# Kernel tuning notes

Hardware: AMD Instinct MI355X
Metric: run time of the kernel (lower is better)

Reference implementation:

```python
import jax, jax.numpy as jnp
import numpy as np

ALPHA = 1.0
NEG = -1e20  # matches torch code's -1e+20 padding for impossible cells


def setup_inputs() -> dict:
    key = jax.random.key(0)
    W = jax.random.normal(key, (32, 512, 1024), dtype=jnp.float32)
    return {"W": W}


def _combine(x, y):
    # associative operator for the log-space linear recurrence
    # m_j = logaddexp(m_{j-1} + a_j, b_j)
    a1, b1 = x
    a2, b2 = y
    return (a1 + a2, jnp.logaddexp(b1 + a2, b2))


def _forward(W):
    # Faithful to BayesianDTW.compute_location / compute_location_new:
    #   mu[:,0,:] = mu[:,:,0] = -1e20, mu[:,0,0] = 0
    #   mu[i,j] = logsumexp(mu[i-1,j], mu[i,j-1], mu[i-1,j-1]) + alpha*W[i-1,j-1]
    # Implemented as a row scan; the within-row left-neighbor dependency is a
    # log-space linear recurrence solved with an associative scan (O(Na*log Nb)
    # depth instead of O(Na*Nb) sequential steps).
    B, Na, Nb = W.shape
    aW = ALPHA * W  # [B, Na, Nb]
    row0 = jnp.concatenate(
        [jnp.zeros((B, 1), W.dtype), jnp.full((B, Nb), NEG, W.dtype)], axis=1
    )  # mu[:, 0, :]

    def step(prev_row, w_row):
        # prev_row: mu[:, i-1, :] -> [B, Nb+1]; w_row: alpha*W[:, i-1, :] -> [B, Nb]
        c = jnp.logaddexp(prev_row[:, 1:], prev_row[:, :-1])  # top + top-left
        # mu[i,j] = logaddexp(mu[i,j-1] + w_j, c_j + w_j), mu[i,0] = NEG
        A, Bc = jax.lax.associative_scan(_combine, (w_row, c + w_row), axis=1)
        m = jnp.logaddexp(NEG + A, Bc)  # include mu[i,0] = NEG initial carry
        new_row = jnp.concatenate(
            [jnp.full((m.shape[0], 1), NEG, m.dtype), m], axis=1
        )
        return new_row, new_row

    _, rows = jax.lax.scan(step, row0, jnp.transpose(aW, (1, 0, 2)))  # [Na, B, Nb+1]
    mu = jnp.concatenate([row0[:, None, :], jnp.transpose(rows, (1, 0, 2))], axis=1)
    return mu  # [B, Na+1, Nb+1], scale=False behavior


def reference(W):
    return _forward(W)
```

## Files before the change

### kernel.cpp

```cpp
#include <hip/hip_runtime.h>
#include <stdint.h>
#include <stddef.h>


#define NBATCH  32
#define NA      512
#define NB      1024
#define NSTRIPE 8
#define SW      128
#define CH      8
#define NCHUNK  (NA / CH)
#define LSTR    128
#define OROWS   513
#define OCOLS   1025
#define FSTRIDE 32

#define NEGV    (-1e20f)
#define LOG2E   (1.4426950408889634f)
#define LN2     (0.6931471805599453f)
#define NEG2    (-1.4426950408889634e20f)
#define FLAGTAG 0x5A000000u

#define EXP2F(x) __builtin_amdgcn_exp2f(x)
#define LOG2F(x) __builtin_amdgcn_logf(x)

__device__ __forceinline__ float lse3_2(float a, float b, float c) {
    float m  = fmaxf(fmaxf(a, b), c);
    float md = __builtin_amdgcn_fmed3f(a, b, c);
    float mn = fminf(fminf(a, b), c);
    float ss = 1.0f + EXP2F(md - m) + EXP2F(mn - m);
    return m + LOG2F(ss);
}

__device__ __forceinline__ float rdlane(float v, int l) {
    return __int_as_float(__builtin_amdgcn_readlane(__float_as_int(v), l));
}

__device__ __forceinline__ float lane_shr1(float x, int lane) {
    int xi  = __float_as_int(x);
    int shr = __builtin_amdgcn_update_dpp(0, xi, 0x111, 0xf, 0xf, true);
    float v = __int_as_float(shr);
    float a15 = rdlane(x, 15), a31 = rdlane(x, 31), a47 = rdlane(x, 47);
    v = (lane == 16) ? a15 : v;
    v = (lane == 32) ? a31 : v;
    v = (lane == 48) ? a47 : v;
    return v;
}

__device__ __forceinline__ unsigned int ld_flag(unsigned int* fp) {
    return __hip_atomic_load(fp, __ATOMIC_RELAXED, __HIP_MEMORY_SCOPE_AGENT);
}
__device__ __forceinline__ void st_flag(unsigned int* fp, unsigned int v) {
    __hip_atomic_store(fp, v, __ATOMIC_RELAXED, __HIP_MEMORY_SCOPE_AGENT);
}
__device__ __forceinline__ float ld_edge(const float* p) {
    return __hip_atomic_load((float*)p, __ATOMIC_RELAXED, __HIP_MEMORY_SCOPE_AGENT);
}
__device__ __forceinline__ void st_edge(float* p, float v) {
    __hip_atomic_store(p, v, __ATOMIC_RELAXED, __HIP_MEMORY_SCOPE_AGENT);
}

__device__ __forceinline__ void wait_flag(unsigned int* fp, unsigned int need) {
    for (int k = 0; k < (1 << 22); ++k) {
        unsigned int v = ld_flag(fp);
        if ((v >> 24) == 0x5Au && (v & 0x00FFFFFFu) >= need) break;
    }
    asm volatile("" ::: "memory");
}

__global__ __launch_bounds__(64, 1)
void dtw_pipe(const float* __restrict__ W, float* __restrict__ out,
              unsigned int* __restrict__ flags)
{
    __shared__ float lds_o[128 * LSTR];

    const int lane = (int)threadIdx.x;
    const int bid  = (int)blockIdx.x;
    const int b    = bid & (NBATCH - 1);
    const int s    = bid >> 5;

    const float*  Wb  = W + ((size_t)b * NA) * NB + s * SW;
    float*        ob  = out + (size_t)b * OROWS * OCOLS;
    unsigned int* fmy = flags + (size_t)bid * FSTRIDE;
    unsigned int* fup = flags + (size_t)(bid - NBATCH) * FSTRIDE;

    ob[s * SW + 1 + lane]      = NEGV;
    ob[s * SW + 1 + 64 + lane] = NEGV;
    if (s == 0) {
        if (lane == 0) ob[0] = 0.0f;
        for (int r = lane; r < NA; r += 64)
            ob[(size_t)(r + 1) * OCOLS] = NEGV;
    }

    float2 wr[4];
    #pragma unroll
    for (int k = 0; k < 4; ++k) {
        int rowc = k - lane;
        rowc = rowc < 0 ? 0 : rowc;
        wr[k] = *(const float2*)&Wb[(size_t)rowc * NB + 2 * lane];
    }

    float evcur = -1e30f, evnxt = -1e30f, lres = -1e30f;
    if (s > 0) {
        wait_flag(fup, 1u);
        if (lane < CH)
            evcur = ld_edge(&ob[(size_t)(1 + lane) * OCOLS + s * SW]) * LOG2E;
        wait_flag(fup, 2u);
        if (lane < CH)
            evnxt = ld_edge(&ob[(size_t)(CH + 1 + lane) * OCOLS + s * SW]) * LOG2E;
        wait_flag(fup, 3u);
        if (lane < CH)
            lres  = ld_edge(&ob[(size_t)(2 * CH + 1 + lane) * OCOLS + s * SW]) * LOG2E;
    }

    asm volatile("s_waitcnt vmcnt(0)" ::: "memory");

    float topA = NEG2, topB = NEG2;
    float sh_in = NEG2;
    float tl_reg = NEG2;
    float ev_im1 = (s == 0) ? 0.0f : NEG2;
    unsigned int fpoll = 0;

    auto stepc = [&](int m, int tt, bool GATE, bool GNA) {
        const int t = 8 * m + tt;
        const int r = t - lane;
        if (tt == 1 && s > 0) fpoll = ld_flag(fup);
        const float2 wv = wr[tt & 3];
        {
            int rowc = r + 4;
            rowc = rowc < 0 ? 0 : (rowc > NA - 1 ? NA - 1 : rowc);
            wr[tt & 3] = *(const float2*)&Wb[(size_t)rowc * NB + 2 * lane];
        }
        const float ev_i = rdlane(evcur, tt);
        const float lf = (lane == 0) ? ev_i   : sh_in;
        const float tl = (lane == 0) ? ev_im1 : tl_reg;
        const float uA = fmaf(wv.x, LOG2E, lse3_2(topA, lf, tl));
        const float uB = fmaf(wv.y, LOG2E, lse3_2(topB, uA, topA));
        bool db = true;
        if (GATE) db = (r >= 0);
        if (GNA)  db = (r < NA);
        if (db) {
            *(float2*)&lds_o[(r & 127) * LSTR + 2 * lane]
                = make_float2(uA * LN2, uB * LN2);
        }
        if (GATE) {
            const bool on = (r >= 0);
            topA   = on ? uA : NEG2;
            topB   = on ? uB : NEG2;
            tl_reg = on ? lf : NEG2;
        } else {
            topA = uA; topB = uB; tl_reg = lf;
        }
        ev_im1 = ev_i;
        sh_in  = lane_shr1(uB, lane);
    };

    auto boundary = [&](int m) {
        const int f = m - 8;
        if (s < NSTRIPE - 1 && f >= 0 && lane < CH) {
            const int rw = (f << 3) + lane;
            const float evl = lds_o[(rw & 127) * LSTR + 127];
            st_edge(ob + (size_t)(rw + 1) * OCOLS + (s + 1) * SW, evl);
        }
        asm volatile("s_waitcnt vmcnt(4)" ::: "memory");
        if (s < NSTRIPE - 1 && f >= 1 && lane == 0)
            st_flag(fmy, FLAGTAG + (unsigned)f);
        if (f >= 0) {
            #pragma unroll
            for (int rr = 0; rr < CH; ++rr) {
                const int rw = (f << 3) + rr;
                const float v0 = lds_o[(rw & 127) * LSTR + lane];
                const float v1 = lds_o[(rw & 127) * LSTR + 64 + lane];
                float* orow = ob + (size_t)(rw + 1) * OCOLS + s * SW + 1;
                orow[lane]      = v0;
                orow[64 + lane] = v1;
            }
        }
        evcur = evnxt; evnxt = lres;
        const int c = m + 3;
        if (s > 0 && c < NCHUNK) {
            const unsigned need = (unsigned)(m + 4);
            if (!((fpoll >> 24) == 0x5Au && (fpoll & 0x00FFFFFFu) >= need))
                wait_flag(fup, need);
            lres = -1e30f;
            if (lane < CH)
                lres = ld_edge(&ob[(size_t)((c << 3) + 1 + lane) * OCOLS + s * SW])
                       * LOG2E;
        }
    };

    for (int m = 0; m < 8; ++m) {
        #pragma unroll
        for (int tt = 0; tt < 8; ++tt) stepc(m, tt, true, false);
        boundary(m);
    }
    for (int m = 8; m < 64; ++m) {
        #pragma unroll
        for (int tt = 0; tt < 8; ++tt) stepc(m, tt, false, false);
        boundary(m);
    }
    for (int m = 64; m < 71; ++m) {
        #pragma unroll
        for (int tt = 0; tt < 8; ++tt) stepc(m, tt, false, true);
        boundary(m);
    }
    #pragma unroll
    for (int tt = 0; tt < 7; ++tt) stepc(71, tt, false, true);

    {
        const int f = NCHUNK - 1;
        if (s < NSTRIPE - 1 && lane < CH) {
            const int rw = (f << 3) + lane;
            const float evl = lds_o[(rw & 127) * LSTR + 127];
            st_edge(ob + (size_t)(rw + 1) * OCOLS + (s + 1) * SW, evl);
        }
        asm volatile("s_waitcnt vmcnt(1)" ::: "memory");
        if (s < NSTRIPE - 1 && lane == 0)
            st_flag(fmy, FLAGTAG + (unsigned)f);
        #pragma unroll
        for (int rr = 0; rr < CH; ++rr) {
            const int rw = (f << 3) + rr;
            const float v0 = lds_o[(rw & 127) * LSTR + lane];
            const float v1 = lds_o[(rw & 127) * LSTR + 64 + lane];
            float* orow = ob + (size_t)(rw + 1) * OCOLS + s * SW + 1;
            orow[lane]      = v0;
            orow[64 + lane] = v1;
        }
        asm volatile("s_waitcnt vmcnt(0)" ::: "memory");
        if (s < NSTRIPE - 1 && lane == 0)
            st_flag(fmy, FLAGTAG + (unsigned)NCHUNK);
    }
}

extern "C" void kernel_launch(void* const* d_in, const int* in_sizes, int n_in,
                              void* d_out, int out_size, void* d_ws, size_t ws_size,
                              hipStream_t stream) {
    const float*  W     = (const float*)d_in[0];
    float*        out   = (float*)d_out;
    unsigned int* flags = (unsigned int*)d_ws;
    (void)in_sizes; (void)n_in; (void)out_size; (void)ws_size;
    hipLaunchKernelGGL(dtw_pipe, dim3(NBATCH * NSTRIPE), dim3(64), 0, stream,
                       W, out, flags);
}
```

Measured before the change: 417.7 us.

## Carry log-sum-exp state as (exponent, mantissa) pair to drop log from recurrence

Replaces the per-cell log-sum-exp with a split representation: a base-2 offset p and a linear-scale factor q. The log2 leaves the serial dependency chain and is only evaluated when storing the output, and q is renormalized by moving its float exponent into p with integer bit operations. The cost is more exp2 calls per cell (three per cell instead of two), extra multiplies and bit manipulation, and two lane shifts per step instead of one. This adds instructions and register pressure, and the readlane-based shift is now done twice.

```diff
diff --git a/kernel.cpp b/kernel.cpp
--- a/kernel.cpp
+++ b/kernel.cpp
@@ -24,14 +24,6 @@
 #define EXP2F(x) __builtin_amdgcn_exp2f(x)
 #define LOG2F(x) __builtin_amdgcn_logf(x)
 
-__device__ __forceinline__ float lse3_2(float a, float b, float c) {
-    float m  = fmaxf(fmaxf(a, b), c);
-    float md = __builtin_amdgcn_fmed3f(a, b, c);
-    float mn = fminf(fminf(a, b), c);
-    float ss = 1.0f + EXP2F(md - m) + EXP2F(mn - m);
-    return m + LOG2F(ss);
-}
-
 __device__ __forceinline__ float rdlane(float v, int l) {
     return __int_as_float(__builtin_amdgcn_readlane(__float_as_int(v), l));
 }
@@ -115,9 +107,10 @@
 
     asm volatile("s_waitcnt vmcnt(0)" ::: "memory");
 
-    float topA = NEG2, topB = NEG2;
-    float sh_in = NEG2;
-    float tl_reg = NEG2;
+    float pA = NEG2, qA = 1.0f;
+    float pB = NEG2, qB = 1.0f;
+    float tlp = NEG2, tlq = 1.0f;
+    float shp = NEG2, shq = 1.0f;
     float ev_im1 = (s == 0) ? 0.0f : NEG2;
     unsigned int fpoll = 0;
 
@@ -132,27 +125,53 @@
             wr[tt & 3] = *(const float2*)&Wb[(size_t)rowc * NB + 2 * lane];
         }
         const float ev_i = rdlane(evcur, tt);
-        const float lf = (lane == 0) ? ev_i   : sh_in;
-        const float tl = (lane == 0) ? ev_im1 : tl_reg;
-        const float uA = fmaf(wv.x, LOG2E, lse3_2(topA, lf, tl));
-        const float uB = fmaf(wv.y, LOG2E, lse3_2(topB, uA, topA));
+        const bool l0 = (lane == 0);
+        const float lfp = l0 ? ev_i   : shp;
+        const float lfq = l0 ? 1.0f   : shq;
+        const float tpp = l0 ? ev_im1 : tlp;
+        const float tpq = l0 ? 1.0f   : tlq;
+        const float m1  = fmaxf(fmaxf(pA, lfp), tpp);
+        const float qAn = qA  * EXP2F(pA  - m1)
+                        + lfq * EXP2F(lfp - m1)
+                        + tpq * EXP2F(tpp - m1);
+        const float pAn = fmaf(wv.x, LOG2E, m1);
+        const float m2  = fmaxf(fmaxf(pB, pAn), pA);
+        const float qBn = qB  * EXP2F(pB  - m2)
+                        + qAn * EXP2F(pAn - m2)
+                        + qA  * EXP2F(pA  - m2);
+        const float pBn = fmaf(wv.y, LOG2E, m2);
         bool db = true;
         if (GATE) db = (r >= 0);
         if (GNA)  db = (r < NA);
         if (db) {
+            const float lnA = (pAn + LOG2F(qAn)) * LN2;
+            const float lnB = (pBn + LOG2F(qBn)) * LN2;
             *(float2*)&lds_o[(r & 127) * LSTR + 2 * lane]
-                = make_float2(uA * LN2, uB * LN2);
+                = make_float2(lnA, lnB);
+        }
+        float pAr = pAn, qAr, pBr = pBn, qBr;
+        {   const int qi = __float_as_int(qAn);
+            const int e  = ((qi >> 23) & 0xff) - 127;
+            pAr += (float)e;
+            qAr  = __int_as_float(qi - (e << 23));
+        }
+        {   const int qi = __float_as_int(qBn);
+            const int e  = ((qi >> 23) & 0xff) - 127;
+            pBr += (float)e;
+            qBr  = __int_as_float(qi - (e << 23));
         }
         if (GATE) {
             const bool on = (r >= 0);
-            topA   = on ? uA : NEG2;
-            topB   = on ? uB : NEG2;
-            tl_reg = on ? lf : NEG2;
+            pA  = on ? pAr : NEG2;  qA  = on ? qAr : 1.0f;
+            pB  = on ? pBr : NEG2;  qB  = on ? qBr : 1.0f;
+            tlp = on ? lfp : NEG2;  tlq = on ? lfq : 1.0f;
         } else {
-            topA = uA; topB = uB; tl_reg = lf;
+            pA = pAr; qA = qAr; pB = pBr; qB = qBr;
+            tlp = lfp; tlq = lfq;
         }
         ev_im1 = ev_i;
-        sh_in  = lane_shr1(uB, lane);
+        shp = lane_shr1(pBr, lane);
+        shq = lane_shr1(qBr, lane);
     };
 
     auto boundary = [&](int m) {
```

New measurement: 467.5 us. 11.9% more time.

## Widen stripes to 256 columns with four cells per lane

Applied to the files above, without the earlier changes.

Halves the number of column stripes per batch, from 8 to 4, so each lane computes four consecutive cells per anti-diagonal step instead of two. W loads and LDS writes widen to float4, and the LDS row buffer moves to dynamically sized shared memory with a padded stride. The aim is to cut the number of inter-stripe handoffs and the pipeline fill lag between stripes. In exchange, the serial per-step logsumexp chain doubles, only half as many blocks run, the LDS footprint grows, and the output writes become strided scalar stores.

```diff
diff --git a/kernel.cpp b/kernel.cpp
--- a/kernel.cpp
+++ b/kernel.cpp
@@ -6,11 +6,11 @@
 #define NBATCH  32
 #define NA      512
 #define NB      1024
-#define NSTRIPE 8
-#define SW      128
+#define NSTRIPE 4
+#define SW      256
 #define CH      8
 #define NCHUNK  (NA / CH)
-#define LSTR    128
+#define LSTR    260
 #define OROWS   513
 #define OCOLS   1025
 #define FSTRIDE 32
@@ -72,7 +72,7 @@
 void dtw_pipe(const float* __restrict__ W, float* __restrict__ out,
               unsigned int* __restrict__ flags)
 {
-    __shared__ float lds_o[128 * LSTR];
+    extern __shared__ float lds_o[];
 
     const int lane = (int)threadIdx.x;
     const int bid  = (int)blockIdx.x;
@@ -84,20 +84,21 @@
     unsigned int* fmy = flags + (size_t)bid * FSTRIDE;
     unsigned int* fup = flags + (size_t)(bid - NBATCH) * FSTRIDE;
 
-    ob[s * SW + 1 + lane]      = NEGV;
-    ob[s * SW + 1 + 64 + lane] = NEGV;
+    #pragma unroll
+    for (int k = 0; k < 4; ++k)
+        ob[s * SW + 1 + 4 * lane + k] = NEGV;
     if (s == 0) {
         if (lane == 0) ob[0] = 0.0f;
         for (int r = lane; r < NA; r += 64)
             ob[(size_t)(r + 1) * OCOLS] = NEGV;
     }
 
-    float2 wr[4];
+    float4 wr[4];
     #pragma unroll
     for (int k = 0; k < 4; ++k) {
         int rowc = k - lane;
         rowc = rowc < 0 ? 0 : rowc;
-        wr[k] = *(const float2*)&Wb[(size_t)rowc * NB + 2 * lane];
+        wr[k] = *(const float4*)&Wb[(size_t)rowc * NB + 4 * lane];
     }
 
     float evcur = -1e30f, evnxt = -1e30f, lres = -1e30f;
@@ -115,7 +116,7 @@
 
     asm volatile("s_waitcnt vmcnt(0)" ::: "memory");
 
-    float topA = NEG2, topB = NEG2;
+    float top0 = NEG2, top1 = NEG2, top2 = NEG2, top3 = NEG2;
     float sh_in = NEG2;
     float tl_reg = NEG2;
     float ev_im1 = (s == 0) ? 0.0f : NEG2;
@@ -125,41 +126,43 @@
         const int t = 8 * m + tt;
         const int r = t - lane;
         if (tt == 1 && s > 0) fpoll = ld_flag(fup);
-        const float2 wv = wr[tt & 3];
+        const float4 wv = wr[tt & 3];
         {
             int rowc = r + 4;
             rowc = rowc < 0 ? 0 : (rowc > NA - 1 ? NA - 1 : rowc);
-            wr[tt & 3] = *(const float2*)&Wb[(size_t)rowc * NB + 2 * lane];
+            wr[tt & 3] = *(const float4*)&Wb[(size_t)rowc * NB + 4 * lane];
         }
         const float ev_i = rdlane(evcur, tt);
         const float lf = (lane == 0) ? ev_i   : sh_in;
         const float tl = (lane == 0) ? ev_im1 : tl_reg;
-        const float uA = fmaf(wv.x, LOG2E, lse3_2(topA, lf, tl));
-        const float uB = fmaf(wv.y, LOG2E, lse3_2(topB, uA, topA));
+        const float u0 = fmaf(wv.x, LOG2E, lse3_2(top0, lf, tl));
+        const float u1 = fmaf(wv.y, LOG2E, lse3_2(top1, u0, top0));
+        const float u2 = fmaf(wv.z, LOG2E, lse3_2(top2, u1, top1));
+        const float u3 = fmaf(wv.w, LOG2E, lse3_2(top3, u2, top2));
         bool db = true;
         if (GATE) db = (r >= 0);
         if (GNA)  db = (r < NA);
         if (db) {
-            *(float2*)&lds_o[(r & 127) * LSTR + 2 * lane]
-                = make_float2(uA * LN2, uB * LN2);
+            *(float4*)&lds_o[(r & 127) * LSTR + 4 * lane]
+                = make_float4(u0 * LN2, u1 * LN2, u2 * LN2, u3 * LN2);
         }
         if (GATE) {
             const bool on = (r >= 0);
-            topA   = on ? uA : NEG2;
-            topB   = on ? uB : NEG2;
+            top0 = on ? u0 : NEG2;  top1 = on ? u1 : NEG2;
+            top2 = on ? u2 : NEG2;  top3 = on ? u3 : NEG2;
             tl_reg = on ? lf : NEG2;
         } else {
-            topA = uA; topB = uB; tl_reg = lf;
+            top0 = u0; top1 = u1; top2 = u2; top3 = u3; tl_reg = lf;
         }
         ev_im1 = ev_i;
-        sh_in  = lane_shr1(uB, lane);
+        sh_in  = lane_shr1(u3, lane);
     };
 
     auto boundary = [&](int m) {
         const int f = m - 8;
         if (s < NSTRIPE - 1 && f >= 0 && lane < CH) {
             const int rw = (f << 3) + lane;
-            const float evl = lds_o[(rw & 127) * LSTR + 127];
+            const float evl = lds_o[(rw & 127) * LSTR + (SW - 1)];
             st_edge(ob + (size_t)(rw + 1) * OCOLS + (s + 1) * SW, evl);
         }
         asm volatile("s_waitcnt vmcnt(4)" ::: "memory");
@@ -169,11 +172,11 @@
             #pragma unroll
             for (int rr = 0; rr < CH; ++rr) {
                 const int rw = (f << 3) + rr;
-                const float v0 = lds_o[(rw & 127) * LSTR + lane];
-                const float v1 = lds_o[(rw & 127) * LSTR + 64 + lane];
-                float* orow = ob + (size_t)(rw + 1) * OCOLS + s * SW + 1;
-                orow[lane]      = v0;
-                orow[64 + lane] = v1;
+                const float4 v = *(const float4*)
+                    &lds_o[(rw & 127) * LSTR + 4 * lane];
+                float* orow = ob + (size_t)(rw + 1) * OCOLS + s * SW + 1
+                            + 4 * lane;
+                orow[0] = v.x; orow[1] = v.y; orow[2] = v.z; orow[3] = v.w;
             }
         }
         evcur = evnxt; evnxt = lres;
@@ -211,7 +214,7 @@
         const int f = NCHUNK - 1;
         if (s < NSTRIPE - 1 && lane < CH) {
             const int rw = (f << 3) + lane;
-            const float evl = lds_o[(rw & 127) * LSTR + 127];
+            const float evl = lds_o[(rw & 127) * LSTR + (SW - 1)];
             st_edge(ob + (size_t)(rw + 1) * OCOLS + (s + 1) * SW, evl);
         }
         asm volatile("s_waitcnt vmcnt(1)" ::: "memory");
@@ -220,11 +223,11 @@
         #pragma unroll
         for (int rr = 0; rr < CH; ++rr) {
             const int rw = (f << 3) + rr;
-            const float v0 = lds_o[(rw & 127) * LSTR + lane];
-            const float v1 = lds_o[(rw & 127) * LSTR + 64 + lane];
-            float* orow = ob + (size_t)(rw + 1) * OCOLS + s * SW + 1;
-            orow[lane]      = v0;
-            orow[64 + lane] = v1;
+            const float4 v = *(const float4*)
+                &lds_o[(rw & 127) * LSTR + 4 * lane];
+            float* orow = ob + (size_t)(rw + 1) * OCOLS + s * SW + 1
+                        + 4 * lane;
+            orow[0] = v.x; orow[1] = v.y; orow[2] = v.z; orow[3] = v.w;
         }
         asm volatile("s_waitcnt vmcnt(0)" ::: "memory");
         if (s < NSTRIPE - 1 && lane == 0)
@@ -239,6 +242,7 @@
     float*        out   = (float*)d_out;
     unsigned int* flags = (unsigned int*)d_ws;
     (void)in_sizes; (void)n_in; (void)out_size; (void)ws_size;
-    hipLaunchKernelGGL(dtw_pipe, dim3(NBATCH * NSTRIPE), dim3(64), 0, stream,
+    hipLaunchKernelGGL(dtw_pipe, dim3(NBATCH * NSTRIPE), dim3(64),
+                       128 * LSTR * sizeof(float), stream,
                        W, out, flags);
 }
```

Result: faster. 391.9 us (-6.2%).
